# Optimization experiments

Hardware: AMD Instinct MI355X
Metric: run time of the kernel (lower is better)

The kernel has to match this reference:

```python
import jax, jax.numpy as jnp
import numpy as np

N = 50000      # num nodes
E = 800000     # num edges (avg degree 16)
DIN = 128
DH = 128
DO = 128
BN_EPS = 1e-5


def setup_inputs() -> dict:
    key = jax.random.key(0)
    ks = jax.random.split(key, 16)
    def lin(k, i, o):
        kw, kb = jax.random.split(k)
        s = 1.0 / np.sqrt(i)
        return (jax.random.uniform(kw, (i, o), jnp.float32, -s, s),
                jax.random.uniform(kb, (o,), jnp.float32, -s, s))
    w0_1, b0_1 = lin(ks[0], DIN, DH)
    w0_2, b0_2 = lin(ks[1], DH, DH)
    w1_1, b1_1 = lin(ks[2], DH, DH)
    w1_2, b1_2 = lin(ks[3], DH, DH)
    w2_1, b2_1 = lin(ks[4], DH, DH)
    w2_2, b2_2 = lin(ks[5], DH, DO)
    return {
        "x": jax.random.normal(ks[6], (N, DIN), jnp.float32),
        "edge_index": jax.random.randint(ks[7], (2, E), 0, N, jnp.int64),
        "eps": jnp.zeros((1,), jnp.float32),
        "w0_1": w0_1, "b0_1": b0_1,
        "bn0_g": jnp.ones((DH,), jnp.float32), "bn0_b": jnp.zeros((DH,), jnp.float32),
        "w0_2": w0_2, "b0_2": b0_2,
        "n0_g": jnp.ones((DH,), jnp.float32), "n0_b": jnp.zeros((DH,), jnp.float32),
        "w1_1": w1_1, "b1_1": b1_1, "w1_2": w1_2, "b1_2": b1_2,
        "n1_g": jnp.ones((DH,), jnp.float32), "n1_b": jnp.zeros((DH,), jnp.float32),
        "w2_1": w2_1, "b2_1": b2_1, "w2_2": w2_2, "b2_2": b2_2,
        "n2_g": jnp.ones((DO,), jnp.float32), "n2_b": jnp.zeros((DO,), jnp.float32),
    }


def _bn(h, g, b):
    # BatchNorm1d in training mode: biased batch statistics over nodes
    m = h.mean(0)
    v = jnp.var(h, axis=0)
    return (h - m) * jax.lax.rsqrt(v + BN_EPS) * g + b


def reference(x, edge_index, eps, w0_1, b0_1, bn0_g, bn0_b, w0_2, b0_2, n0_g, n0_b,
              w1_1, b1_1, w1_2, b1_2, n1_g, n1_b,
              w2_1, b2_1, w2_2, b2_2, n2_g, n2_b):
    src, dst = edge_index[0], edge_index[1]

    def agg(h):
        # GIN aggregation: (1+eps)*x_i + sum_{j in N(i)} x_j
        msg = jax.ops.segment_sum(h[src], dst, num_segments=N)
        return (1.0 + eps) * h + msg

    # Layer 0: MLP = Linear -> BN -> ReLU -> Linear, then outer BN + ReLU
    h = agg(x)
    h = h @ w0_1 + b0_1
    h = jax.nn.relu(_bn(h, bn0_g, bn0_b))
    h = h @ w0_2 + b0_2
    h = jax.nn.relu(_bn(h, n0_g, n0_b))

    # Layer 1: MLP = Linear -> ReLU -> Linear, then BN + ReLU
    h = agg(h)
    h = jax.nn.relu(h @ w1_1 + b1_1)
    h = h @ w1_2 + b1_2
    h = jax.nn.relu(_bn(h, n1_g, n1_b))

    # Layer 2: MLP = Linear -> ReLU -> Linear(dim_o), then BN + ReLU
    h = agg(h)
    h = jax.nn.relu(h @ w2_1 + b2_1)
    h = h @ w2_2 + b2_2
    h = jax.nn.relu(_bn(h, n2_g, n2_b))
    return h
```

## Files before the change

kernel.cpp:

```cpp
#include <hip/hip_runtime.h>


typedef __bf16 bf16x8_t __attribute__((ext_vector_type(8)));
typedef float f32x4_t __attribute__((ext_vector_type(4)));
typedef unsigned short u16x8_t __attribute__((ext_vector_type(8)));
typedef unsigned short u16x4_t __attribute__((ext_vector_type(4)));

__device__ __forceinline__ unsigned short f2bf(float f) {
  unsigned u = __builtin_bit_cast(unsigned, f);
  u += 0x7FFFu + ((u >> 16) & 1u);
  return (unsigned short)(u >> 16);
}
__device__ __forceinline__ float bf2f(unsigned short h) {
  unsigned u = ((unsigned)h) << 16;
  return __builtin_bit_cast(float, u);
}

__global__ __launch_bounds__(256) void k_bcount(const int* __restrict__ dst,
                                                unsigned* __restrict__ tot,
                                                int E, int nb) {
  __shared__ unsigned c[256];
  c[threadIdx.x] = 0;
  __syncthreads();
  for (int e = blockIdx.x * 256 + threadIdx.x; e < E; e += gridDim.x * 256)
    atomicAdd(&c[dst[e] >> 8], 1u);
  __syncthreads();
  int t = threadIdx.x;
  if (t < nb && c[t]) atomicAdd(&tot[t], c[t]);
}

__global__ void k_bscan(const unsigned* __restrict__ tot, unsigned* __restrict__ base,
                        unsigned* __restrict__ fill, float* __restrict__ stats, int nb) {
  __shared__ unsigned s[256];
  int t = threadIdx.x;
  for (int i = t; i < 1024; i += 256) stats[i] = 0.f;
  s[t] = (t < nb) ? tot[t] : 0u;
  __syncthreads();
  for (int o = 1; o < 256; o <<= 1) {
    unsigned u = (t >= o) ? s[t - o] : 0u;
    __syncthreads();
    s[t] += u;
    __syncthreads();
  }
  unsigned excl = t ? s[t - 1] : 0u;
  if (t < nb) {
    base[t] = excl;
    fill[t] = excl;
  }
  if (t == nb) base[t] = s[nb - 1];
}

__global__ __launch_bounds__(256) void k_bucket(const int* __restrict__ src,
                                                const int* __restrict__ dst,
                                                unsigned* __restrict__ bucket_fill,
                                                unsigned* __restrict__ ebuf,
                                                int E, int nb, int chunk) {
  __shared__ unsigned cntl[256];
  __shared__ unsigned basel[256];
  __shared__ unsigned fill2[256];
  const int t = threadIdx.x;
  cntl[t] = 0;
  fill2[t] = 0;
  __syncthreads();
  const int lo = blockIdx.x * chunk;
  const int hi = (lo + chunk < E) ? lo + chunk : E;
  for (int e = lo + t; e < hi; e += 256)
    atomicAdd(&cntl[dst[e] >> 8], 1u);
  __syncthreads();
  if (t < nb) basel[t] = atomicAdd(&bucket_fill[t], cntl[t]);
  __syncthreads();
  for (int e = lo + t; e < hi; e += 256) {
    int d = dst[e];
    int b = d >> 8;
    unsigned slot = atomicAdd(&fill2[b], 1u);
    ebuf[basel[b] + slot] = ((unsigned)(d & 255) << 24) | (unsigned)src[e];
  }
}

__global__ __launch_bounds__(256) void k_build(const unsigned* __restrict__ ebuf,
                                               const unsigned* __restrict__ bucket_base,
                                               unsigned* __restrict__ csr_off,
                                               int* __restrict__ csr, int N) {
  __shared__ unsigned cntl[256];
  __shared__ unsigned scl[256];
  __shared__ unsigned startl[256];
  __shared__ unsigned filll[256];
  const int b = blockIdx.x;
  const int t = threadIdx.x;
  const unsigned ebeg = bucket_base[b];
  const unsigned eend = bucket_base[b + 1];
  cntl[t] = 0;
  filll[t] = 0;
  __syncthreads();
  for (unsigned e = ebeg + t; e < eend; e += 256)
    atomicAdd(&cntl[ebuf[e] >> 24], 1u);
  __syncthreads();
  unsigned v = cntl[t];
  scl[t] = v;
  __syncthreads();
  for (int o = 1; o < 256; o <<= 1) {
    unsigned u = (t >= o) ? scl[t - o] : 0u;
    __syncthreads();
    scl[t] += u;
    __syncthreads();
  }
  int node = b * 256 + t;
  if (node < N) csr_off[node] = ebeg + scl[t];
  startl[t] = scl[t] - v;
  __syncthreads();
  for (unsigned e = ebeg + t; e < eend; e += 256) {
    unsigned p = ebuf[e];
    unsigned d = p >> 24;
    unsigned slot = atomicAdd(&filll[d], 1u);
    csr[ebeg + startl[d] + slot] = (int)(p & 0xFFFFFFu);
  }
}

__global__ void k_wtx(const float* w0, const float* w1, const float* w2,
                      const float* w3, const float* w4, const float* w5,
                      unsigned short* __restrict__ wT,
                      const float* __restrict__ x, unsigned short* __restrict__ xb,
                      int total8) {
  if (blockIdx.x < 96) {
    const float* ws[6] = {w0, w1, w2, w3, w4, w5};
    int m = blockIdx.x >> 4;
    int tl = blockIdx.x & 15;
    int tr = (tl >> 2) * 32;
    int tc = (tl & 3) * 32;
    const float* W = ws[m];
    __shared__ float sm[32][33];
    int r = threadIdx.x >> 3;
    int c4 = (threadIdx.x & 7) * 4;
    float4 v = *reinterpret_cast<const float4*>(&W[(tr + r) * 128 + tc + c4]);
    sm[r][c4 + 0] = v.x; sm[r][c4 + 1] = v.y; sm[r][c4 + 2] = v.z; sm[r][c4 + 3] = v.w;
    __syncthreads();
    u16x4_t o;
    o[0] = f2bf(sm[c4 + 0][r]);
    o[1] = f2bf(sm[c4 + 1][r]);
    o[2] = f2bf(sm[c4 + 2][r]);
    o[3] = f2bf(sm[c4 + 3][r]);
    *reinterpret_cast<u16x4_t*>(&wT[(size_t)m * 16384 + (tc + r) * 128 + tr + c4]) = o;
  } else {
    int i = (blockIdx.x - 96) * 256 + threadIdx.x;
    if (i >= total8) return;
    const float* p = x + (size_t)i * 8;
    float4 f0 = *reinterpret_cast<const float4*>(p);
    float4 f1 = *reinterpret_cast<const float4*>(p + 4);
    u16x8_t o;
    o[0] = f2bf(f0.x); o[1] = f2bf(f0.y); o[2] = f2bf(f0.z); o[3] = f2bf(f0.w);
    o[4] = f2bf(f1.x); o[5] = f2bf(f1.y); o[6] = f2bf(f1.z); o[7] = f2bf(f1.w);
    *reinterpret_cast<u16x8_t*>(xb + (size_t)i * 8) = o;
  }
}

template<int MODE>
__global__ __launch_bounds__(256) void k_agg(
    const unsigned short* __restrict__ Zv, const float* __restrict__ Zself,
    const float* __restrict__ ssum, const float* __restrict__ ssq,
    const float* __restrict__ gg, const float* __restrict__ bb,
    const int* __restrict__ csr, const unsigned* __restrict__ offend,
    const float* __restrict__ epsp, unsigned short* __restrict__ out, int N) {
  __shared__ float scl[128], shl[128];
  const int tid = threadIdx.x;
  if (MODE == 1) {
    if (tid < 128) {
      float inv = 1.f / (float)N;
      float m = ssum[tid] * inv;
      float vv = ssq[tid] * inv - m * m;
      float s = gg[tid] * rsqrtf(vv + 1e-5f);
      scl[tid] = s;
      shl[tid] = bb[tid] - m * s;
    }
    __syncthreads();
  }
  int node = blockIdx.x * 4 + (tid >> 6);
  if (node >= N) return;
  const int lane = tid & 63;
  const int sub = lane >> 4;
  const int t = lane & 15;
  const int c0 = t * 8;

  float sc[8], sh[8];
  if (MODE == 1) {
#pragma unroll
    for (int j = 0; j < 8; ++j) { sc[j] = scl[c0 + j]; sh[j] = shl[c0 + j]; }
  }

  float s[8];
#pragma unroll
  for (int j = 0; j < 8; ++j) s[j] = 0.f;

  auto accum = [&](int row) {
    u16x8_t v = *reinterpret_cast<const u16x8_t*>(Zv + (size_t)row * 128 + c0);
    if (MODE == 0) {
#pragma unroll
      for (int j = 0; j < 8; ++j) s[j] += bf2f(v[j]);
    } else {
#pragma unroll
      for (int j = 0; j < 8; ++j) s[j] += fmaxf(bf2f(v[j]) * sc[j] + sh[j], 0.f);
    }
  };

  const unsigned beg = node ? offend[node - 1] : 0u;
  const unsigned end = offend[node];
  const int deg = (int)(end - beg);
  const int deg64 = deg < 64 ? deg : 64;

  int idx = (lane < deg64) ? csr[beg + lane] : 0;

  const int nIter = (deg64 + 3) >> 2;
  int p = sub;
  int i = 0;
  for (; i + 4 <= nIter; i += 4, p += 16) {
    int r0 = __shfl(idx, p);
    int r1 = __shfl(idx, p + 4);
    int r2 = __shfl(idx, p + 8);
    int r3 = __shfl(idx, p + 12);
    if (p < deg64) accum(r0);
    if (p + 4 < deg64) accum(r1);
    if (p + 8 < deg64) accum(r2);
    if (p + 12 < deg64) accum(r3);
  }
  for (; i < nIter; ++i, p += 4) {
    int r0 = __shfl(idx, p);
    if (p < deg64) accum(r0);
  }

  for (int e = 64 + sub; e < deg; e += 4) accum(csr[beg + e]);

  if (sub == 0) {
    float ep = 1.f + epsp[0];
    if (MODE == 0) {
      const float* Z = Zself + (size_t)node * 128 + c0;
      float4 f0 = *reinterpret_cast<const float4*>(Z);
      float4 f1 = *reinterpret_cast<const float4*>(Z + 4);
      s[0] += ep * f0.x; s[1] += ep * f0.y; s[2] += ep * f0.z; s[3] += ep * f0.w;
      s[4] += ep * f1.x; s[5] += ep * f1.y; s[6] += ep * f1.z; s[7] += ep * f1.w;
    } else {
      u16x8_t v = *reinterpret_cast<const u16x8_t*>(Zv + (size_t)node * 128 + c0);
#pragma unroll
      for (int j = 0; j < 8; ++j)
        s[j] += ep * fmaxf(bf2f(v[j]) * sc[j] + sh[j], 0.f);
    }
  }

#pragma unroll
  for (int j = 0; j < 8; ++j) {
    s[j] += __shfl_xor(s[j], 16);
    s[j] += __shfl_xor(s[j], 32);
  }

  if (sub == 0) {
    u16x8_t o;
#pragma unroll
    for (int j = 0; j < 8; ++j) o[j] = f2bf(s[j]);
    *reinterpret_cast<u16x8_t*>(out + (size_t)node * 128 + c0) = o;
  }
}

template<bool IN_BN, bool OUT_RELU, bool STATS>
__global__ __launch_bounds__(256) void k_mm(
    const unsigned short* __restrict__ A,
    const float* __restrict__ ssum, const float* __restrict__ ssq,
    const float* __restrict__ gg, const float* __restrict__ bb,
    const unsigned short* __restrict__ BT, const float* __restrict__ bias,
    unsigned short* __restrict__ Y, float* __restrict__ osum, float* __restrict__ osq,
    int M, int N) {
  __shared__ __attribute__((aligned(16))) unsigned short Bl[128][136];
  __shared__ float cs[128], cq[128];
  __shared__ float scl[128], shl[128];
  const int tid = threadIdx.x;
  const int r0 = blockIdx.x * 128;
  const int trow = tid >> 4;
  const int tch = (tid & 15) * 8;

#pragma unroll
  for (int pass = 0; pass < 8; ++pass) {
    int n = pass * 16 + trow;
    u16x8_t v = *reinterpret_cast<const u16x8_t*>(&BT[(size_t)n * 128 + tch]);
    *reinterpret_cast<u16x8_t*>(&Bl[n][tch]) = v;
  }
  if (IN_BN && tid < 128) {
    float inv = 1.f / (float)N;
    float m = ssum[tid] * inv;
    float vv = ssq[tid] * inv - m * m;
    float s = gg[tid] * rsqrtf(vv + 1e-5f);
    scl[tid] = s;
    shl[tid] = bb[tid] - m * s;
  }
  if (STATS && tid < 128) { cs[tid] = 0.f; cq[tid] = 0.f; }

  const int wave = tid >> 6;
  const int lane = tid & 63;
  const int lr = lane & 15;
  const int lkb = (lane >> 4) * 8;
  const int wr = r0 + wave * 32;

  u16x8_t araw[2][4];
  const u16x8_t zv = {0, 0, 0, 0, 0, 0, 0, 0};
#pragma unroll
  for (int mr = 0; mr < 2; ++mr) {
    int grow = wr + mr * 16 + lr;
    bool ok = grow < M;
    const unsigned short* Ar = A + (size_t)grow * 128 + lkb;
#pragma unroll
    for (int kc = 0; kc < 4; ++kc)
      araw[mr][kc] = ok ? *reinterpret_cast<const u16x8_t*>(Ar + kc * 32) : zv;
  }
  __syncthreads();

  if (IN_BN) {
#pragma unroll
    for (int kc = 0; kc < 4; ++kc) {
      float scv[8], shv[8];
#pragma unroll
      for (int j = 0; j < 8; ++j) {
        int c = kc * 32 + lkb + j;
        scv[j] = scl[c]; shv[j] = shl[c];
      }
#pragma unroll
      for (int mr = 0; mr < 2; ++mr) {
#pragma unroll
        for (int j = 0; j < 8; ++j)
          araw[mr][kc][j] = f2bf(fmaxf(bf2f(araw[mr][kc][j]) * scv[j] + shv[j], 0.f));
      }
    }
  }

  f32x4_t acc[2][8];
  f32x4_t zero = {0.f, 0.f, 0.f, 0.f};
#pragma unroll
  for (int mr = 0; mr < 2; ++mr)
#pragma unroll
    for (int i = 0; i < 8; ++i) acc[mr][i] = zero;

#pragma unroll
  for (int kc = 0; kc < 4; ++kc) {
    bf16x8_t a0 = __builtin_bit_cast(bf16x8_t, araw[0][kc]);
    bf16x8_t a1 = __builtin_bit_cast(bf16x8_t, araw[1][kc]);
#pragma unroll
    for (int nt = 0; nt < 8; ++nt) {
      bf16x8_t bf = __builtin_bit_cast(bf16x8_t,
          *reinterpret_cast<const u16x8_t*>(&Bl[nt * 16 + lr][kc * 32 + lkb]));
      acc[0][nt] = __builtin_amdgcn_mfma_f32_16x16x32_bf16(a0, bf, acc[0][nt], 0, 0, 0);
      acc[1][nt] = __builtin_amdgcn_mfma_f32_16x16x32_bf16(a1, bf, acc[1][nt], 0, 0, 0);
    }
  }

  const int g = lane >> 4;
#pragma unroll
  for (int mr = 0; mr < 2; ++mr) {
#pragma unroll
    for (int nt = 0; nt < 8; ++nt) {
      int col = nt * 16 + lr;
      float bv = bias[col];
      float s4 = 0.f, q4 = 0.f;
#pragma unroll
      for (int j = 0; j < 4; ++j) {
        int gr = wr + mr * 16 + g * 4 + j;
        float v = acc[mr][nt][j] + bv;
        if (OUT_RELU) v = fmaxf(v, 0.f);
        if (gr < M) {
          Y[(size_t)gr * 128 + col] = f2bf(v);
          if (STATS) { s4 += v; q4 += v * v; }
        }
      }
      if (STATS) {
        s4 += __shfl_xor(s4, 16);
        s4 += __shfl_xor(s4, 32);
        q4 += __shfl_xor(q4, 16);
        q4 += __shfl_xor(q4, 32);
        if (lane < 16) { atomicAdd(&cs[col], s4); atomicAdd(&cq[col], q4); }
      }
    }
  }
  if (STATS) {
    __syncthreads();
    if (tid < 128) {
      atomicAdd(&osum[tid], cs[tid]);
      atomicAdd(&osq[tid], cq[tid]);
    }
  }
}

__global__ __launch_bounds__(256) void k_mm2x(
    const unsigned short* __restrict__ A,
    const unsigned short* __restrict__ BT1, const float* __restrict__ bias1,
    const unsigned short* __restrict__ BT2, const float* __restrict__ bias2,
    unsigned short* __restrict__ Y, float* __restrict__ osum, float* __restrict__ osq,
    int M) {
  __shared__ __attribute__((aligned(16))) unsigned short Al[128][136];
  __shared__ __attribute__((aligned(16))) unsigned short Bl[128][136];
  __shared__ float cs[128], cq[128];
  const int tid = threadIdx.x;
  const int r0 = blockIdx.x * 128;
  const int trow = tid >> 4;
  const int tch = (tid & 15) * 8;

#pragma unroll
  for (int pass = 0; pass < 8; ++pass) {
    int n = pass * 16 + trow;
    u16x8_t v = *reinterpret_cast<const u16x8_t*>(&BT1[(size_t)n * 128 + tch]);
    *reinterpret_cast<u16x8_t*>(&Bl[n][tch]) = v;
  }
  if (tid < 128) { cs[tid] = 0.f; cq[tid] = 0.f; }

  const int wave = tid >> 6;
  const int lane = tid & 63;
  const int lr = lane & 15;
  const int lkb = (lane >> 4) * 8;
  const int wr = r0 + wave * 32;
  const int g = lane >> 4;

  u16x8_t araw[2][4];
  const u16x8_t zv = {0, 0, 0, 0, 0, 0, 0, 0};
#pragma unroll
  for (int mr = 0; mr < 2; ++mr) {
    int grow = wr + mr * 16 + lr;
    bool ok = grow < M;
    const unsigned short* Ar = A + (size_t)grow * 128 + lkb;
#pragma unroll
    for (int kc = 0; kc < 4; ++kc)
      araw[mr][kc] = ok ? *reinterpret_cast<const u16x8_t*>(Ar + kc * 32) : zv;
  }
  __syncthreads();

  f32x4_t acc[2][8];
  f32x4_t zero = {0.f, 0.f, 0.f, 0.f};
#pragma unroll
  for (int mr = 0; mr < 2; ++mr)
#pragma unroll
    for (int i = 0; i < 8; ++i) acc[mr][i] = zero;

#pragma unroll
  for (int kc = 0; kc < 4; ++kc) {
    bf16x8_t a0 = __builtin_bit_cast(bf16x8_t, araw[0][kc]);
    bf16x8_t a1 = __builtin_bit_cast(bf16x8_t, araw[1][kc]);
#pragma unroll
    for (int nt = 0; nt < 8; ++nt) {
      bf16x8_t bf = __builtin_bit_cast(bf16x8_t,
          *reinterpret_cast<const u16x8_t*>(&Bl[nt * 16 + lr][kc * 32 + lkb]));
      acc[0][nt] = __builtin_amdgcn_mfma_f32_16x16x32_bf16(a0, bf, acc[0][nt], 0, 0, 0);
      acc[1][nt] = __builtin_amdgcn_mfma_f32_16x16x32_bf16(a1, bf, acc[1][nt], 0, 0, 0);
    }
  }
  __syncthreads();

#pragma unroll
  for (int pass = 0; pass < 8; ++pass) {
    int n = pass * 16 + trow;
    u16x8_t v = *reinterpret_cast<const u16x8_t*>(&BT2[(size_t)n * 128 + tch]);
    *reinterpret_cast<u16x8_t*>(&Bl[n][tch]) = v;
  }
#pragma unroll
  for (int mr = 0; mr < 2; ++mr) {
#pragma unroll
    for (int nt = 0; nt < 8; ++nt) {
      int col = nt * 16 + lr;
      float bv = bias1[col];
#pragma unroll
      for (int j = 0; j < 4; ++j) {
        Al[wave * 32 + mr * 16 + g * 4 + j][col] = f2bf(fmaxf(acc[mr][nt][j] + bv, 0.f));
      }
    }
  }
  __syncthreads();

#pragma unroll
  for (int mr = 0; mr < 2; ++mr)
#pragma unroll
    for (int i = 0; i < 8; ++i) acc[mr][i] = zero;
#pragma unroll
  for (int kc = 0; kc < 4; ++kc) {
    bf16x8_t a0 = __builtin_bit_cast(bf16x8_t,
        *reinterpret_cast<const u16x8_t*>(&Al[wave * 32 + lr][kc * 32 + lkb]));
    bf16x8_t a1 = __builtin_bit_cast(bf16x8_t,
        *reinterpret_cast<const u16x8_t*>(&Al[wave * 32 + 16 + lr][kc * 32 + lkb]));
#pragma unroll
    for (int nt = 0; nt < 8; ++nt) {
      bf16x8_t bf = __builtin_bit_cast(bf16x8_t,
          *reinterpret_cast<const u16x8_t*>(&Bl[nt * 16 + lr][kc * 32 + lkb]));
      acc[0][nt] = __builtin_amdgcn_mfma_f32_16x16x32_bf16(a0, bf, acc[0][nt], 0, 0, 0);
      acc[1][nt] = __builtin_amdgcn_mfma_f32_16x16x32_bf16(a1, bf, acc[1][nt], 0, 0, 0);
    }
  }

#pragma unroll
  for (int mr = 0; mr < 2; ++mr) {
#pragma unroll
    for (int nt = 0; nt < 8; ++nt) {
      int col = nt * 16 + lr;
      float bv = bias2[col];
      float s4 = 0.f, q4 = 0.f;
#pragma unroll
      for (int j = 0; j < 4; ++j) {
        int gr = wr + mr * 16 + g * 4 + j;
        float v = acc[mr][nt][j] + bv;
        if (gr < M) {
          Y[(size_t)gr * 128 + col] = f2bf(v);
          s4 += v; q4 += v * v;
        }
      }
      s4 += __shfl_xor(s4, 16);
      s4 += __shfl_xor(s4, 32);
      q4 += __shfl_xor(q4, 16);
      q4 += __shfl_xor(q4, 32);
      if (lane < 16) { atomicAdd(&cs[col], s4); atomicAdd(&cq[col], q4); }
    }
  }
  __syncthreads();
  if (tid < 128) {
    atomicAdd(&osum[tid], cs[tid]);
    atomicAdd(&osq[tid], cq[tid]);
  }
}

__global__ void k_final(const unsigned short* __restrict__ Y,
                        const float* __restrict__ ssum, const float* __restrict__ ssq,
                        const float* __restrict__ gg, const float* __restrict__ bb,
                        float* __restrict__ out, int total8, int N) {
  __shared__ float scl[128], shl[128];
  const int tid = threadIdx.x;
  if (tid < 128) {
    float inv = 1.f / (float)N;
    float m = ssum[tid] * inv;
    float vv = ssq[tid] * inv - m * m;
    float s = gg[tid] * rsqrtf(vv + 1e-5f);
    scl[tid] = s;
    shl[tid] = bb[tid] - m * s;
  }
  __syncthreads();
  int i = blockIdx.x * 256 + tid;
  if (i >= total8) return;
  int base = i * 8;
  int c = base & 127;
  u16x8_t v = *reinterpret_cast<const u16x8_t*>(&Y[base]);
  float4 o0, o1;
  o0.x = fmaxf(bf2f(v[0]) * scl[c + 0] + shl[c + 0], 0.f);
  o0.y = fmaxf(bf2f(v[1]) * scl[c + 1] + shl[c + 1], 0.f);
  o0.z = fmaxf(bf2f(v[2]) * scl[c + 2] + shl[c + 2], 0.f);
  o0.w = fmaxf(bf2f(v[3]) * scl[c + 3] + shl[c + 3], 0.f);
  o1.x = fmaxf(bf2f(v[4]) * scl[c + 4] + shl[c + 4], 0.f);
  o1.y = fmaxf(bf2f(v[5]) * scl[c + 5] + shl[c + 5], 0.f);
  o1.z = fmaxf(bf2f(v[6]) * scl[c + 6] + shl[c + 6], 0.f);
  o1.w = fmaxf(bf2f(v[7]) * scl[c + 7] + shl[c + 7], 0.f);
  *reinterpret_cast<float4*>(&out[base]) = o0;
  *reinterpret_cast<float4*>(&out[base + 4]) = o1;
}

extern "C" void kernel_launch(void* const* d_in, const int* in_sizes, int n_in,
                              void* d_out, int out_size, void* d_ws, size_t ws_size,
                              hipStream_t stream) {
  (void)n_in; (void)out_size; (void)ws_size;
  const float* x = (const float*)d_in[0];
  const int* ei = (const int*)d_in[1];
  const float* eps = (const float*)d_in[2];
  const int N = in_sizes[0] / 128;
  const int E = in_sizes[1] / 2;
  const int* src = ei;
  const int* dst = ei + E;

  char* ws = (char*)d_ws;
  size_t off = 0;
  auto alloc = [&](size_t bytes) -> char* {
    char* p = ws + off;
    off += (bytes + 255) & ~(size_t)255;
    return p;
  };
  unsigned* csr_off = (unsigned*)alloc((size_t)N * 4);
  int* csr_src = (int*)alloc((size_t)E * 4);
  unsigned* bucket_tot = (unsigned*)alloc(256 * 4);
  unsigned* bucket_base = (unsigned*)alloc(257 * 4);
  unsigned* bucket_fill = (unsigned*)alloc(256 * 4);
  float* stats = (float*)alloc(8 * 128 * 4);
  unsigned short* wT = (unsigned short*)alloc(6 * 128 * 128 * 2);
  unsigned short* xb = (unsigned short*)alloc((size_t)N * 128 * 2);
  unsigned short* B1 = (unsigned short*)alloc((size_t)N * 128 * 2);
  unsigned short* B2 = (unsigned short*)alloc((size_t)N * 128 * 2);
  unsigned* ebuf = (unsigned*)B1;

  hipMemsetAsync(bucket_tot, 0, 256 * 4, stream);

  const int NBUCK = (N + 255) >> 8;
  const int gA = (N + 3) / 4;
  const int gM = (N + 127) / 128;
  const int gF = ((N * 128 / 8) + 255) / 256;
  const int chunk = (E + 255) / 256;

  k_bcount<<<256, 256, 0, stream>>>(dst, bucket_tot, E, NBUCK);
  k_bscan<<<1, 256, 0, stream>>>(bucket_tot, bucket_base, bucket_fill, stats, NBUCK);
  k_bucket<<<256, 256, 0, stream>>>(src, dst, bucket_fill, ebuf, E, NBUCK, chunk);
  k_build<<<NBUCK, 256, 0, stream>>>(ebuf, bucket_base, csr_off, csr_src, N);
  k_wtx<<<96 + gF, 256, 0, stream>>>((const float*)d_in[3], (const float*)d_in[7],
                                     (const float*)d_in[11], (const float*)d_in[13],
                                     (const float*)d_in[17], (const float*)d_in[19], wT,
                                     x, xb, N * 128 / 8);

  k_agg<0><<<gA, 256, 0, stream>>>(xb, x, nullptr, nullptr, nullptr, nullptr,
                                   csr_src, csr_off, eps, B1, N);
  k_mm<false, false, true><<<gM, 256, 0, stream>>>(B1, nullptr, nullptr, nullptr, nullptr,
      wT + 0 * 16384, (const float*)d_in[4], B2, stats + 0, stats + 128, N, N);
  k_mm<true, false, true><<<gM, 256, 0, stream>>>(B2, stats + 0, stats + 128,
      (const float*)d_in[5], (const float*)d_in[6],
      wT + 1 * 16384, (const float*)d_in[8], B1, stats + 256, stats + 384, N, N);

  k_agg<1><<<gA, 256, 0, stream>>>(B1, nullptr, stats + 256, stats + 384,
                                   (const float*)d_in[9], (const float*)d_in[10],
                                   csr_src, csr_off, eps, B2, N);
  k_mm2x<<<gM, 256, 0, stream>>>(B2, wT + 2 * 16384, (const float*)d_in[12],
      wT + 3 * 16384, (const float*)d_in[14], B1, stats + 512, stats + 640, N);

  k_agg<1><<<gA, 256, 0, stream>>>(B1, nullptr, stats + 512, stats + 640,
                                   (const float*)d_in[15], (const float*)d_in[16],
                                   csr_src, csr_off, eps, B2, N);
  k_mm2x<<<gM, 256, 0, stream>>>(B2, wT + 4 * 16384, (const float*)d_in[18],
      wT + 5 * 16384, (const float*)d_in[20], B1, stats + 768, stats + 896, N);

  k_final<<<gF, 256, 0, stream>>>(B1, stats + 768, stats + 896,
                                  (const float*)d_in[21], (const float*)d_in[22],
                                  (float*)d_out, N * 128 / 8, N);
}
```

Before: 270.7 us.

## Store CSR source indices as 16-bit and split GEMM rows across 8 waves

CSR source indices are now stored as unsigned 16-bit values, which halves index traffic in the three aggregation passes. Because N is 50000, every index fits in 16 bits, but larger graphs would silently break. The matmul kernels now launch with 512 threads, so each of 8 waves handles 16 rows instead of 32 per 128-row tile. This lowers per-wave register use and should raise latency hiding, at the cost of less reuse of each B fragment per LDS read.

Result: faster. 264.6 us (-2.2%).

```diff
diff --git a/kernel.cpp b/kernel.cpp
--- a/kernel.cpp
+++ b/kernel.cpp
@@ -80,7 +80,7 @@
 __global__ __launch_bounds__(256) void k_build(const unsigned* __restrict__ ebuf,
                                                const unsigned* __restrict__ bucket_base,
                                                unsigned* __restrict__ csr_off,
-                                               int* __restrict__ csr, int N) {
+                                               unsigned short* __restrict__ csr, int N) {
   __shared__ unsigned cntl[256];
   __shared__ unsigned scl[256];
   __shared__ unsigned startl[256];
@@ -112,7 +112,7 @@
     unsigned p = ebuf[e];
     unsigned d = p >> 24;
     unsigned slot = atomicAdd(&filll[d], 1u);
-    csr[ebeg + startl[d] + slot] = (int)(p & 0xFFFFFFu);
+    csr[ebeg + startl[d] + slot] = (unsigned short)(p & 0xFFFFu);
   }
 }
 
@@ -158,7 +158,7 @@
     const unsigned short* __restrict__ Zv, const float* __restrict__ Zself,
     const float* __restrict__ ssum, const float* __restrict__ ssq,
     const float* __restrict__ gg, const float* __restrict__ bb,
-    const int* __restrict__ csr, const unsigned* __restrict__ offend,
+    const unsigned short* __restrict__ csr, const unsigned* __restrict__ offend,
     const float* __restrict__ epsp, unsigned short* __restrict__ out, int N) {
   __shared__ float scl[128], shl[128];
   const int tid = threadIdx.x;
@@ -206,7 +206,7 @@
   const int deg = (int)(end - beg);
   const int deg64 = deg < 64 ? deg : 64;
 
-  int idx = (lane < deg64) ? csr[beg + lane] : 0;
+  int idx = (lane < deg64) ? (int)csr[beg + lane] : 0;
 
   const int nIter = (deg64 + 3) >> 2;
   int p = sub;
@@ -226,7 +226,7 @@
     if (p < deg64) accum(r0);
   }
 
-  for (int e = 64 + sub; e < deg; e += 4) accum(csr[beg + e]);
+  for (int e = 64 + sub; e < deg; e += 4) accum((int)csr[beg + e]);
 
   if (sub == 0) {
     float ep = 1.f + epsp[0];
@@ -259,7 +259,7 @@
 }
 
 template<bool IN_BN, bool OUT_RELU, bool STATS>
-__global__ __launch_bounds__(256) void k_mm(
+__global__ __launch_bounds__(512) void k_mm(
     const unsigned short* __restrict__ A,
     const float* __restrict__ ssum, const float* __restrict__ ssq,
     const float* __restrict__ gg, const float* __restrict__ bb,
@@ -275,10 +275,10 @@
   const int tch = (tid & 15) * 8;
 
 #pragma unroll
-  for (int pass = 0; pass < 8; ++pass) {
-    int n = pass * 16 + trow;
-    u16x8_t v = *reinterpret_cast<const u16x8_t*>(&BT[(size_t)n * 128 + tch]);
-    *reinterpret_cast<u16x8_t*>(&Bl[n][tch]) = v;
+  for (int pass = 0; pass < 4; ++pass) {
+    int n = pass * 32 + trow;
+    *reinterpret_cast<u16x8_t*>(&Bl[n][tch]) =
+        *reinterpret_cast<const u16x8_t*>(&BT[(size_t)n * 128 + tch]);
   }
   if (IN_BN && tid < 128) {
     float inv = 1.f / (float)N;
@@ -294,84 +294,69 @@
   const int lane = tid & 63;
   const int lr = lane & 15;
   const int lkb = (lane >> 4) * 8;
-  const int wr = r0 + wave * 32;
-
-  u16x8_t araw[2][4];
+  const int wr = r0 + wave * 16;
+
+  u16x8_t araw[4];
   const u16x8_t zv = {0, 0, 0, 0, 0, 0, 0, 0};
-#pragma unroll
-  for (int mr = 0; mr < 2; ++mr) {
-    int grow = wr + mr * 16 + lr;
+  {
+    int grow = wr + lr;
     bool ok = grow < M;
     const unsigned short* Ar = A + (size_t)grow * 128 + lkb;
 #pragma unroll
     for (int kc = 0; kc < 4; ++kc)
-      araw[mr][kc] = ok ? *reinterpret_cast<const u16x8_t*>(Ar + kc * 32) : zv;
+      araw[kc] = ok ? *reinterpret_cast<const u16x8_t*>(Ar + kc * 32) : zv;
   }
   __syncthreads();
 
   if (IN_BN) {
 #pragma unroll
     for (int kc = 0; kc < 4; ++kc) {
-      float scv[8], shv[8];
 #pragma unroll
       for (int j = 0; j < 8; ++j) {
         int c = kc * 32 + lkb + j;
-        scv[j] = scl[c]; shv[j] = shl[c];
+        araw[kc][j] = f2bf(fmaxf(bf2f(araw[kc][j]) * scl[c] + shl[c], 0.f));
       }
-#pragma unroll
-      for (int mr = 0; mr < 2; ++mr) {
-#pragma unroll
-        for (int j = 0; j < 8; ++j)
-          araw[mr][kc][j] = f2bf(fmaxf(bf2f(araw[mr][kc][j]) * scv[j] + shv[j], 0.f));
-      }
-    }
-  }
-
-  f32x4_t acc[2][8];
+    }
+  }
+
+  f32x4_t acc[8];
   f32x4_t zero = {0.f, 0.f, 0.f, 0.f};
 #pragma unroll
-  for (int mr = 0; mr < 2; ++mr)
-#pragma unroll
-    for (int i = 0; i < 8; ++i) acc[mr][i] = zero;
+  for (int i = 0; i < 8; ++i) acc[i] = zero;
 
 #pragma unroll
   for (int kc = 0; kc < 4; ++kc) {
-    bf16x8_t a0 = __builtin_bit_cast(bf16x8_t, araw[0][kc]);
-    bf16x8_t a1 = __builtin_bit_cast(bf16x8_t, araw[1][kc]);
+    bf16x8_t af = __builtin_bit_cast(bf16x8_t, araw[kc]);
 #pragma unroll
     for (int nt = 0; nt < 8; ++nt) {
       bf16x8_t bf = __builtin_bit_cast(bf16x8_t,
           *reinterpret_cast<const u16x8_t*>(&Bl[nt * 16 + lr][kc * 32 + lkb]));
-      acc[0][nt] = __builtin_amdgcn_mfma_f32_16x16x32_bf16(a0, bf, acc[0][nt], 0, 0, 0);
-      acc[1][nt] = __builtin_amdgcn_mfma_f32_16x16x32_bf16(a1, bf, acc[1][nt], 0, 0, 0);
+      acc[nt] = __builtin_amdgcn_mfma_f32_16x16x32_bf16(af, bf, acc[nt], 0, 0, 0);
     }
   }
 
   const int g = lane >> 4;
 #pragma unroll
-  for (int mr = 0; mr < 2; ++mr) {
-#pragma unroll
-    for (int nt = 0; nt < 8; ++nt) {
-      int col = nt * 16 + lr;
-      float bv = bias[col];
-      float s4 = 0.f, q4 = 0.f;
-#pragma unroll
-      for (int j = 0; j < 4; ++j) {
-        int gr = wr + mr * 16 + g * 4 + j;
-        float v = acc[mr][nt][j] + bv;
-        if (OUT_RELU) v = fmaxf(v, 0.f);
-        if (gr < M) {
-          Y[(size_t)gr * 128 + col] = f2bf(v);
-          if (STATS) { s4 += v; q4 += v * v; }
-        }
+  for (int nt = 0; nt < 8; ++nt) {
+    int col = nt * 16 + lr;
+    float bv = bias[col];
+    float s4 = 0.f, q4 = 0.f;
+#pragma unroll
+    for (int j = 0; j < 4; ++j) {
+      int gr = wr + g * 4 + j;
+      float v = acc[nt][j] + bv;
+      if (OUT_RELU) v = fmaxf(v, 0.f);
+      if (gr < M) {
+        Y[(size_t)gr * 128 + col] = f2bf(v);
+        if (STATS) { s4 += v; q4 += v * v; }
       }
-      if (STATS) {
-        s4 += __shfl_xor(s4, 16);
-        s4 += __shfl_xor(s4, 32);
-        q4 += __shfl_xor(q4, 16);
-        q4 += __shfl_xor(q4, 32);
-        if (lane < 16) { atomicAdd(&cs[col], s4); atomicAdd(&cq[col], q4); }
-      }
+    }
+    if (STATS) {
+      s4 += __shfl_xor(s4, 16);
+      s4 += __shfl_xor(s4, 32);
+      q4 += __shfl_xor(q4, 16);
+      q4 += __shfl_xor(q4, 32);
+      if (lane < 16) { atomicAdd(&cs[col], s4); atomicAdd(&cq[col], q4); }
     }
   }
   if (STATS) {
@@ -383,7 +368,7 @@
   }
 }
 
-__global__ __launch_bounds__(256) void k_mm2x(
+__global__ __launch_bounds__(512) void k_mm2x(
     const unsigned short* __restrict__ A,
     const unsigned short* __restrict__ BT1, const float* __restrict__ bias1,
     const unsigned short* __restrict__ BT2, const float* __restrict__ bias2,
@@ -398,10 +383,10 @@
   const int tch = (tid & 15) * 8;
 
 #pragma unroll
-  for (int pass = 0; pass < 8; ++pass) {
-    int n = pass * 16 + trow;
-    u16x8_t v = *reinterpret_cast<const u16x8_t*>(&BT1[(size_t)n * 128 + tch]);
-    *reinterpret_cast<u16x8_t*>(&Bl[n][tch]) = v;
+  for (int pass = 0; pass < 4; ++pass) {
+    int n = pass * 32 + trow;
+    *reinterpret_cast<u16x8_t*>(&Bl[n][tch]) =
+        *reinterpret_cast<const u16x8_t*>(&BT1[(size_t)n * 128 + tch]);
   }
   if (tid < 128) { cs[tid] = 0.f; cq[tid] = 0.f; }
 
@@ -409,104 +394,89 @@
   const int lane = tid & 63;
   const int lr = lane & 15;
   const int lkb = (lane >> 4) * 8;
-  const int wr = r0 + wave * 32;
+  const int wr = r0 + wave * 16;
   const int g = lane >> 4;
 
-  u16x8_t araw[2][4];
+  u16x8_t araw[4];
   const u16x8_t zv = {0, 0, 0, 0, 0, 0, 0, 0};
-#pragma unroll
-  for (int mr = 0; mr < 2; ++mr) {
-    int grow = wr + mr * 16 + lr;
+  {
+    int grow = wr + lr;
     bool ok = grow < M;
     const unsigned short* Ar = A + (size_t)grow * 128 + lkb;
 #pragma unroll
     for (int kc = 0; kc < 4; ++kc)
-      araw[mr][kc] = ok ? *reinterpret_cast<const u16x8_t*>(Ar + kc * 32) : zv;
-  }
-  __syncthreads();
-
-  f32x4_t acc[2][8];
+      araw[kc] = ok ? *reinterpret_cast<const u16x8_t*>(Ar + kc * 32) : zv;
+  }
+  __syncthreads();
+
+  f32x4_t acc[8];
   f32x4_t zero = {0.f, 0.f, 0.f, 0.f};
 #pragma unroll
-  for (int mr = 0; mr < 2; ++mr)
-#pragma unroll
-    for (int i = 0; i < 8; ++i) acc[mr][i] = zero;
+  for (int i = 0; i < 8; ++i) acc[i] = zero;
 
 #pragma unroll
   for (int kc = 0; kc < 4; ++kc) {
-    bf16x8_t a0 = __builtin_bit_cast(bf16x8_t, araw[0][kc]);
-    bf16x8_t a1 = __builtin_bit_cast(bf16x8_t, araw[1][kc]);
+    bf16x8_t af = __builtin_bit_cast(bf16x8_t, araw[kc]);
 #pragma unroll
     for (int nt = 0; nt < 8; ++nt) {
       bf16x8_t bf = __builtin_bit_cast(bf16x8_t,
           *reinterpret_cast<const u16x8_t*>(&Bl[nt * 16 + lr][kc * 32 + lkb]));
-      acc[0][nt] = __builtin_amdgcn_mfma_f32_16x16x32_bf16(a0, bf, acc[0][nt], 0, 0, 0);
-      acc[1][nt] = __builtin_amdgcn_mfma_f32_16x16x32_bf16(a1, bf, acc[1][nt], 0, 0, 0);
-    }
-  }
-  __syncthreads();
-
-#pragma unroll
-  for (int pass = 0; pass < 8; ++pass) {
-    int n = pass * 16 + trow;
-    u16x8_t v = *reinterpret_cast<const u16x8_t*>(&BT2[(size_t)n * 128 + tch]);
-    *reinterpret_cast<u16x8_t*>(&Bl[n][tch]) = v;
-  }
-#pragma unroll
-  for (int mr = 0; mr < 2; ++mr) {
-#pragma unroll
-    for (int nt = 0; nt < 8; ++nt) {
-      int col = nt * 16 + lr;
-      float bv = bias1[col];
-#pragma unroll
-      for (int j = 0; j < 4; ++j) {
-        Al[wave * 32 + mr * 16 + g * 4 + j][col] = f2bf(fmaxf(acc[mr][nt][j] + bv, 0.f));
-      }
-    }
-  }
-  __syncthreads();
-
-#pragma unroll
-  for (int mr = 0; mr < 2; ++mr)
-#pragma unroll
-    for (int i = 0; i < 8; ++i) acc[mr][i] = zero;
+      acc[nt] = __builtin_amdgcn_mfma_f32_16x16x32_bf16(af, bf, acc[nt], 0, 0, 0);
+    }
+  }
+  __syncthreads();
+
+#pragma unroll
+  for (int pass = 0; pass < 4; ++pass) {
+    int n = pass * 32 + trow;
+    *reinterpret_cast<u16x8_t*>(&Bl[n][tch]) =
+        *reinterpret_cast<const u16x8_t*>(&BT2[(size_t)n * 128 + tch]);
+  }
+#pragma unroll
+  for (int nt = 0; nt < 8; ++nt) {
+    int col = nt * 16 + lr;
+    float bv = bias1[col];
+#pragma unroll
+    for (int j = 0; j < 4; ++j)
+      Al[wave * 16 + g * 4 + j][col] = f2bf(fmaxf(acc[nt][j] + bv, 0.f));
+  }
+  __syncthreads();
+
+#pragma unroll
+  for (int kc = 0; kc < 4; ++kc)
+    araw[kc] = *reinterpret_cast<const u16x8_t*>(&Al[wave * 16 + lr][kc * 32 + lkb]);
+#pragma unroll
+  for (int i = 0; i < 8; ++i) acc[i] = zero;
 #pragma unroll
   for (int kc = 0; kc < 4; ++kc) {
-    bf16x8_t a0 = __builtin_bit_cast(bf16x8_t,
-        *reinterpret_cast<const u16x8_t*>(&Al[wave * 32 + lr][kc * 32 + lkb]));
-    bf16x8_t a1 = __builtin_bit_cast(bf16x8_t,
-        *reinterpret_cast<const u16x8_t*>(&Al[wave * 32 + 16 + lr][kc * 32 + lkb]));
+    bf16x8_t af = __builtin_bit_cast(bf16x8_t, araw[kc]);
 #pragma unroll
     for (int nt = 0; nt < 8; ++nt) {
       bf16x8_t bf = __builtin_bit_cast(bf16x8_t,
           *reinterpret_cast<const u16x8_t*>(&Bl[nt * 16 + lr][kc * 32 + lkb]));
-      acc[0][nt] = __builtin_amdgcn_mfma_f32_16x16x32_bf16(a0, bf, acc[0][nt], 0, 0, 0);
-      acc[1][nt] = __builtin_amdgcn_mfma_f32_16x16x32_bf16(a1, bf, acc[1][nt], 0, 0, 0);
-    }
-  }
-
-#pragma unroll
-  for (int mr = 0; mr < 2; ++mr) {
-#pragma unroll
-    for (int nt = 0; nt < 8; ++nt) {
-      int col = nt * 16 + lr;
-      float bv = bias2[col];
-      float s4 = 0.f, q4 = 0.f;
-#pragma unroll
-      for (int j = 0; j < 4; ++j) {
-        int gr = wr + mr * 16 + g * 4 + j;
-        float v = acc[mr][nt][j] + bv;
-        if (gr < M) {
-          Y[(size_t)gr * 128 + col] = f2bf(v);
-          s4 += v; q4 += v * v;
-        }
+      acc[nt] = __builtin_amdgcn_mfma_f32_16x16x32_bf16(af, bf, acc[nt], 0, 0, 0);
+    }
+  }
+
+#pragma unroll
+  for (int nt = 0; nt < 8; ++nt) {
+    int col = nt * 16 + lr;
+    float bv = bias2[col];
+    float s4 = 0.f, q4 = 0.f;
+#pragma unroll
+    for (int j = 0; j < 4; ++j) {
+      int gr = wr + g * 4 + j;
+      float v = acc[nt][j] + bv;
+      if (gr < M) {
+        Y[(size_t)gr * 128 + col] = f2bf(v);
+        s4 += v; q4 += v * v;
       }
-      s4 += __shfl_xor(s4, 16);
-      s4 += __shfl_xor(s4, 32);
-      q4 += __shfl_xor(q4, 16);
-      q4 += __shfl_xor(q4, 32);
-      if (lane < 16) { atomicAdd(&cs[col], s4); atomicAdd(&cq[col], q4); }
-    }
+    }
+    s4 += __shfl_xor(s4, 16);
+    s4 += __shfl_xor(s4, 32);
+    q4 += __shfl_xor(q4, 16);
+    q4 += __shfl_xor(q4, 32);
+    if (lane < 16) { atomicAdd(&cs[col], s4); atomicAdd(&cq[col], q4); }
   }
   __syncthreads();
   if (tid < 128) {
@@ -568,7 +538,7 @@
     return p;
   };
   unsigned* csr_off = (unsigned*)alloc((size_t)N * 4);
-  int* csr_src = (int*)alloc((size_t)E * 4);
+  unsigned short* csr_src = (unsigned short*)alloc((size_t)E * 2);
   unsigned* bucket_tot = (unsigned*)alloc(256 * 4);
   unsigned* bucket_base = (unsigned*)alloc(257 * 4);
   unsigned* bucket_fill = (unsigned*)alloc(256 * 4);
@@ -598,22 +568,22 @@
 
   k_agg<0><<<gA, 256, 0, stream>>>(xb, x, nullptr, nullptr, nullptr, nullptr,
                                    csr_src, csr_off, eps, B1, N);
-  k_mm<false, false, true><<<gM, 256, 0, stream>>>(B1, nullptr, nullptr, nullptr, nullptr,
+  k_mm<false, false, true><<<gM, 512, 0, stream>>>(B1, nullptr, nullptr, nullptr, nullptr,
       wT + 0 * 16384, (const float*)d_in[4], B2, stats + 0, stats + 128, N, N);
-  k_mm<true, false, true><<<gM, 256, 0, stream>>>(B2, stats + 0, stats + 128,
+  k_mm<true, false, true><<<gM, 512, 0, stream>>>(B2, stats + 0, stats + 128,
       (const float*)d_in[5], (const float*)d_in[6],
       wT + 1 * 16384, (const float*)d_in[8], B1, stats + 256, stats + 384, N, N);
 
   k_agg<1><<<gA, 256, 0, stream>>>(B1, nullptr, stats + 256, stats + 384,
                                    (const float*)d_in[9], (const float*)d_in[10],
                                    csr_src, csr_off, eps, B2, N);
-  k_mm2x<<<gM, 256, 0, stream>>>(B2, wT + 2 * 16384, (const float*)d_in[12],
+  k_mm2x<<<gM, 512, 0, stream>>>(B2, wT + 2 * 16384, (const float*)d_in[12],
       wT + 3 * 16384, (const float*)d_in[14], B1, stats + 512, stats + 640, N);
 
   k_agg<1><<<gA, 256, 0, stream>>>(B1, nullptr, stats + 512, stats + 640,
                                    (const float*)d_in[15], (const float*)d_in[16],
                                    csr_src, csr_off, eps, B2, N);
-  k_mm2x<<<gM, 256, 0, stream>>>(B2, wT + 4 * 16384, (const float*)d_in[18],
+  k_mm2x<<<gM, 512, 0, stream>>>(B2, wT + 4 * 16384, (const float*)d_in[18],
       wT + 5 * 16384, (const float*)d_in[20], B1, stats + 768, stats + 896, N);
 
   k_final<<<gF, 256, 0, stream>>>(B1, stats + 768, stats + 896,
```
